# Kernel optimization log

Hardware: AMD Instinct MI355X
Metric: run time of the kernel (lower is better)

The kernel has to match this reference:

```python
import jax, jax.numpy as jnp
import numpy as np

B, S, D_IN, D_HID, D_OUT = 8, 2048, 1024, 1024, 1024


def setup_inputs() -> dict:
    key = jax.random.key(0)
    ks = jax.random.split(key, 11)
    def lin(kw, kb, fan_in, fan_out):
        bound = 1.0 / np.sqrt(fan_in)
        W = jax.random.uniform(kw, (fan_out, fan_in), minval=-bound, maxval=bound, dtype=jnp.float32)
        b = jax.random.uniform(kb, (fan_out,), minval=-bound, maxval=bound, dtype=jnp.float32)
        return W, b
    Wq, bq = lin(ks[0], ks[1], D_IN, D_HID)
    Wk, bk = lin(ks[2], ks[3], D_IN, D_HID)
    Wv, bv = lin(ks[4], ks[5], D_IN, D_HID)
    Wo, bo = lin(ks[6], ks[7], D_HID, D_OUT)
    gamma = jnp.ones((D_OUT,), jnp.float32)
    beta = jnp.zeros((D_OUT,), jnp.float32)
    x = jax.random.normal(ks[8], (B, S, D_IN), dtype=jnp.float32)
    return {"x": x, "Wq": Wq, "bq": bq, "Wk": Wk, "bk": bk,
            "Wv": Wv, "bv": bv, "Wo": Wo, "bo": bo,
            "gamma": gamma, "beta": beta}


def _layer_norm(x, gamma, beta, eps=1e-5):
    mu = jnp.mean(x, axis=-1, keepdims=True)
    var = jnp.var(x, axis=-1, keepdims=True)
    return (x - mu) * jax.lax.rsqrt(var + eps) * gamma + beta


def reference(x, Wq, bq, Wk, bk, Wv, bv, Wo, bo, gamma, beta):
    q = jnp.einsum('bsd,hd->bsh', x, Wq) + bq   # [B,S,H]
    k = jnp.einsum('bsd,hd->bsh', x, Wk) + bk
    v = jnp.einsum('bsd,hd->bsh', x, Wv) + bv
    scale = 1.0 / jnp.sqrt(jnp.float32(D_HID))
    scores = jnp.einsum('bqh,bkh->bqk', q, k) * scale  # [B,S,S]
    attn = jax.nn.softmax(scores, axis=-1)
    weighted = jnp.einsum('bqk,bkh->bqh', attn, v)     # [B,S,H]
    out = jnp.einsum('bsh,oh->bso', weighted, Wo) + bo # [B,S,O]
    return _layer_norm(out + x, gamma, beta)
```

## Files before the change

### kernel.cpp

```cpp
#include <hip/hip_runtime.h>
#include <hip/hip_bf16.h>
#include <math.h>


typedef __bf16 bf16;
typedef unsigned char u8;
typedef __attribute__((ext_vector_type(8))) __bf16 bf16x8;
typedef __attribute__((ext_vector_type(4))) __bf16 bf16x4;
typedef __attribute__((ext_vector_type(8))) int i32x8;
typedef __attribute__((ext_vector_type(16))) float f32x16;

__device__ __forceinline__ void async16(const u8* g, u8* l) {
    __builtin_amdgcn_global_load_lds(
        (const __attribute__((address_space(1))) void*)g,
        (__attribute__((address_space(3))) void*)l, 16, 0, 0);
}

#define WAITCNT_VM(n) __builtin_amdgcn_s_waitcnt((15 << 8) | (7 << 4) | (n))

__device__ __forceinline__ u8 to_fp8(float v) {
    return (u8)(__builtin_amdgcn_cvt_pk_fp8_f32(v, v, 0, 0) & 0xFF);
}

__global__ __launch_bounds__(256) void cast_all(
    const float* __restrict__ x,
    const float* __restrict__ W0, const float* __restrict__ W1,
    const float* __restrict__ W2, const float* __restrict__ W3,
    const float* __restrict__ bq, const float* __restrict__ bk,
    u8* __restrict__ x8, u8* __restrict__ w8, float* __restrict__ bqk)
{
    const int b = blockIdx.x, t = threadIdx.x;
    if (b < 8192) {
        const int i = (b * 256 + t) * 8;
        float4 a = *(const float4*)(x + i);
        float4 c = *(const float4*)(x + i + 4);
        int lo = __builtin_amdgcn_cvt_pk_fp8_f32(a.x, a.y, 0, 0);
        lo = __builtin_amdgcn_cvt_pk_fp8_f32(a.z, a.w, lo, 1);
        int hi = __builtin_amdgcn_cvt_pk_fp8_f32(c.x, c.y, 0, 0);
        hi = __builtin_amdgcn_cvt_pk_fp8_f32(c.z, c.w, hi, 1);
        int2 o = { lo, hi };
        *(int2*)(x8 + i) = o;
    } else if (b < 10240) {
        const int bb = b - 8192;
        const int wsel = bb >> 9;
        const float* src = (wsel == 0) ? W0 : (wsel == 1) ? W1
                         : (wsel == 2) ? W2 : W3;
        const int i = ((bb & 511) * 256 + t) * 8;
        float4 a = *(const float4*)(src + i);
        float4 c = *(const float4*)(src + i + 4);
        int lo = __builtin_amdgcn_cvt_pk_fp8_f32(a.x, a.y, 0, 0);
        lo = __builtin_amdgcn_cvt_pk_fp8_f32(a.z, a.w, lo, 1);
        int hi = __builtin_amdgcn_cvt_pk_fp8_f32(c.x, c.y, 0, 0);
        hi = __builtin_amdgcn_cvt_pk_fp8_f32(c.z, c.w, hi, 1);
        int2 o = { lo, hi };
        *(int2*)(w8 + (size_t)wsel * 1048576 + i) = o;
    } else {
        const int i = t * 8;
        const float* s = (i < 1024) ? (bq + i) : (bk + i - 1024);
        float4 a = *(const float4*)s;
        float4 c = *(const float4*)(s + 4);
        *(float4*)(bqk + i) = a;
        *(float4*)(bqk + i + 4) = c;
    }
}

__global__ __launch_bounds__(512) void gemm_f8(
    const u8* __restrict__ A, long lda, long sA,
    const u8* __restrict__ B, long ldb, long sB,
    void* __restrict__ Cv, long ldc, long sC,
    const float* __restrict__ bias, int bias_mode,
    float scale, int c_mode, int K)
{
    __shared__ u8 lds[3][32768];

    const int gx = gridDim.x, gy = gridDim.y;
    const int slice = gx * gy;
    const int total = slice * gridDim.z;
    int flat = ((int)blockIdx.z * gy + (int)blockIdx.y) * gx + (int)blockIdx.x;
    if ((total & 7) == 0)
        flat = (flat & 7) * (total >> 3) + (flat >> 3);
    const int bz = flat / slice;
    const int rem = flat - bz * slice;
    const int by = rem / gx;
    const int bx = rem - by * gx;

    const int tid = threadIdx.x;
    const long tM = (long)by * 256;
    const long tN = (long)bx * 256;
    A += (long)bz * sA;
    B += (long)bz * sB;

    const int s = tid & 255;
    const int line0 = s >> 3;
    const int sch = (s & 7) ^ (line0 & 7);
    const int skb = (sch & 3) << 4;
    const int srofs = (sch & 4) ? 128 : 0;
    const u8* gsrc;
    long gstr;
    if (tid < 256) { gsrc = A + (tM + line0 + srofs) * lda + skb; gstr = lda; }
    else           { gsrc = B + (tN + line0 + srofs) * ldb + skb; gstr = ldb; }
    const int dbase = ((tid < 256) ? 0 : 16384) + s * 16;

    const int w = tid >> 6, lane = tid & 63;
    const int wr = w >> 2, wc = w & 3;
    const int r32 = lane & 31, kh = lane >> 5;
    const int xr = r32 & 7;

    int oA[4][2], oB[2][2];
    const int cbA = wr * 4;
    const int cbB = (wc >> 1) * 4;
#pragma unroll
    for (int q = 0; q < 4; q++) {
        const int lineA = q * 32 + r32;
        oA[q][0] = lineA * 128 + (((cbA + 2 * kh + 0) ^ xr) << 4);
        oA[q][1] = lineA * 128 + (((cbA + 2 * kh + 1) ^ xr) << 4);
    }
#pragma unroll
    for (int n = 0; n < 2; n++) {
        const int lineB = (wc & 1) * 64 + n * 32 + r32;
        oB[n][0] = 16384 + lineB * 128 + (((cbB + 2 * kh + 0) ^ xr) << 4);
        oB[n][1] = 16384 + lineB * 128 + (((cbB + 2 * kh + 1) ^ xr) << 4);
    }

    f32x16 acc[4][2] = {};

    const int T = K >> 6;

#pragma unroll
    for (int j = 0; j < 4; j++)
        async16(gsrc + (long)j * 32 * gstr, &lds[0][dbase + j * 4096]);
#pragma unroll
    for (int j = 0; j < 4; j++)
        async16(gsrc + 64 + (long)j * 32 * gstr, &lds[1][dbase + j * 4096]);

    union F { i32x8 v; int4 q2[2]; };

    int cur = 0;
    for (int t = 0; t < T; ++t) {
        if (t + 1 < T) WAITCNT_VM(4);
        else WAITCNT_VM(0);
        __builtin_amdgcn_s_barrier();

        const u8* cb = lds[cur];

        F a0, a1, b0, b1;
        a0.q2[0] = *(const int4*)&cb[oA[0][0]];
        a0.q2[1] = *(const int4*)&cb[oA[0][1]];
        a1.q2[0] = *(const int4*)&cb[oA[1][0]];
        a1.q2[1] = *(const int4*)&cb[oA[1][1]];
        b0.q2[0] = *(const int4*)&cb[oB[0][0]];
        b0.q2[1] = *(const int4*)&cb[oB[0][1]];
        b1.q2[0] = *(const int4*)&cb[oB[1][0]];
        b1.q2[1] = *(const int4*)&cb[oB[1][1]];
        __builtin_amdgcn_sched_barrier(0);

        F a2, a3;
        a2.q2[0] = *(const int4*)&cb[oA[2][0]];
        a2.q2[1] = *(const int4*)&cb[oA[2][1]];
        a3.q2[0] = *(const int4*)&cb[oA[3][0]];
        a3.q2[1] = *(const int4*)&cb[oA[3][1]];
        if (t + 2 < T) {
            int nb = cur + 2; if (nb >= 3) nb -= 3;
            u8* pn = lds[nb];
            const long ko = (long)(t + 2) << 6;
#pragma unroll
            for (int j = 0; j < 4; j++)
                async16(gsrc + ko + (long)j * 32 * gstr,
                        pn + dbase + j * 4096);
        }

        asm volatile("s_waitcnt lgkmcnt(4)" ::: "memory");
        __builtin_amdgcn_sched_barrier(0);
        __builtin_amdgcn_s_setprio(1);
        acc[0][0] = __builtin_amdgcn_mfma_scale_f32_32x32x64_f8f6f4(
            a0.v, b0.v, acc[0][0], 0, 0, 0, 0x7F7F7F7F, 0, 0x7F7F7F7F);
        acc[0][1] = __builtin_amdgcn_mfma_scale_f32_32x32x64_f8f6f4(
            a0.v, b1.v, acc[0][1], 0, 0, 0, 0x7F7F7F7F, 0, 0x7F7F7F7F);
        acc[1][0] = __builtin_amdgcn_mfma_scale_f32_32x32x64_f8f6f4(
            a1.v, b0.v, acc[1][0], 0, 0, 0, 0x7F7F7F7F, 0, 0x7F7F7F7F);
        acc[1][1] = __builtin_amdgcn_mfma_scale_f32_32x32x64_f8f6f4(
            a1.v, b1.v, acc[1][1], 0, 0, 0, 0x7F7F7F7F, 0, 0x7F7F7F7F);
        __builtin_amdgcn_s_setprio(0);

        asm volatile("s_waitcnt lgkmcnt(0)" ::: "memory");
        __builtin_amdgcn_sched_barrier(0);
        __builtin_amdgcn_s_setprio(1);
        acc[2][0] = __builtin_amdgcn_mfma_scale_f32_32x32x64_f8f6f4(
            a2.v, b0.v, acc[2][0], 0, 0, 0, 0x7F7F7F7F, 0, 0x7F7F7F7F);
        acc[2][1] = __builtin_amdgcn_mfma_scale_f32_32x32x64_f8f6f4(
            a2.v, b1.v, acc[2][1], 0, 0, 0, 0x7F7F7F7F, 0, 0x7F7F7F7F);
        acc[3][0] = __builtin_amdgcn_mfma_scale_f32_32x32x64_f8f6f4(
            a3.v, b0.v, acc[3][0], 0, 0, 0, 0x7F7F7F7F, 0, 0x7F7F7F7F);
        acc[3][1] = __builtin_amdgcn_mfma_scale_f32_32x32x64_f8f6f4(
            a3.v, b1.v, acc[3][1], 0, 0, 0, 0x7F7F7F7F, 0, 0x7F7F7F7F);
        __builtin_amdgcn_s_setprio(0);

        if (++cur >= 3) cur = 0;
    }

#pragma unroll
    for (int q = 0; q < 4; q++) {
#pragma unroll
        for (int n = 0; n < 2; n++) {
            const long gn = tN + wc * 64 + n * 32 + r32;
            const float bn = (bias_mode == 1) ? bias[gn] : 0.0f;
#pragma unroll
            for (int reg = 0; reg < 16; reg++) {
                const int rowf = (reg & 3) + 8 * (reg >> 2) + 4 * kh;
                const long gm = tM + wr * 128 + q * 32 + rowf;
                float v = acc[q][n][reg] * scale + bn;
                if (bias_mode == 2) v += bias[gm];
                if (c_mode == 0)
                    ((bf16*)Cv + (long)bz * sC)[gm * ldc + gn] = (bf16)v;
                else
                    ((u8*)Cv + (long)bz * sC)[gm * ldc + gn] = to_fp8(v);
            }
        }
    }
}

__global__ __launch_bounds__(256) void softmax_f8(
    const bf16* __restrict__ S, u8* __restrict__ P)
{
    const long row = blockIdx.x;
    const bf16* p = S + row * 2048;
    const int t = threadIdx.x;

    bf16x8 v = *(const bf16x8*)(p + t * 8);
    float f[8];
    float m = -3.0e38f;
#pragma unroll
    for (int i = 0; i < 8; i++) { f[i] = (float)v[i]; m = fmaxf(m, f[i]); }
    for (int o = 32; o; o >>= 1) m = fmaxf(m, __shfl_down(m, o));

    __shared__ float sm[4], ssum[4];
    if ((t & 63) == 0) sm[t >> 6] = m;
    __syncthreads();
    m = fmaxf(fmaxf(sm[0], sm[1]), fmaxf(sm[2], sm[3]));

    float s = 0.0f;
#pragma unroll
    for (int i = 0; i < 8; i++) { f[i] = __expf(f[i] - m); s += f[i]; }
    for (int o = 32; o; o >>= 1) s += __shfl_down(s, o);
    if ((t & 63) == 0) ssum[t >> 6] = s;
    __syncthreads();
    s = ssum[0] + ssum[1] + ssum[2] + ssum[3];

    const float c = 256.0f / s;
    int lo = __builtin_amdgcn_cvt_pk_fp8_f32(f[0] * c, f[1] * c, 0, 0);
    lo = __builtin_amdgcn_cvt_pk_fp8_f32(f[2] * c, f[3] * c, lo, 1);
    int hi = __builtin_amdgcn_cvt_pk_fp8_f32(f[4] * c, f[5] * c, 0, 0);
    hi = __builtin_amdgcn_cvt_pk_fp8_f32(f[6] * c, f[7] * c, hi, 1);
    int2 o = { lo, hi };
    *(int2*)(P + row * 2048 + t * 8) = o;
}

__global__ __launch_bounds__(256) void ln_res(
    const bf16* __restrict__ pre, const float* __restrict__ x,
    const float* __restrict__ gamma, const float* __restrict__ beta,
    float* __restrict__ out)
{
    const long row = blockIdx.x;
    const int t = threadIdx.x;
    const long base = row * 1024 + t * 4;

    bf16x4 a = *(const bf16x4*)(pre + base);
    float4 b = *(const float4*)(x + base);
    float v0 = (float)a[0] + b.x, v1 = (float)a[1] + b.y;
    float v2 = (float)a[2] + b.z, v3 = (float)a[3] + b.w;

    float s = v0 + v1 + v2 + v3;
    float q = v0 * v0 + v1 * v1 + v2 * v2 + v3 * v3;
    for (int o = 32; o; o >>= 1) { s += __shfl_down(s, o); q += __shfl_down(q, o); }

    __shared__ float ls[4], lq[4];
    if ((t & 63) == 0) { ls[t >> 6] = s; lq[t >> 6] = q; }
    __syncthreads();
    s = ls[0] + ls[1] + ls[2] + ls[3];
    q = lq[0] + lq[1] + lq[2] + lq[3];

    const float mean = s * (1.0f / 1024.0f);
    const float var = q * (1.0f / 1024.0f) - mean * mean;
    const float rstd = rsqrtf(var + 1e-5f);

    const int c = t * 4;
    float4 g = *(const float4*)(gamma + c);
    float4 be = *(const float4*)(beta + c);
    float4 o;
    o.x = (v0 - mean) * rstd * g.x + be.x;
    o.y = (v1 - mean) * rstd * g.y + be.y;
    o.z = (v2 - mean) * rstd * g.z + be.z;
    o.w = (v3 - mean) * rstd * g.w + be.w;
    *(float4*)(out + base) = o;
}

extern "C" void kernel_launch(void* const* d_in, const int* in_sizes, int n_in,
                              void* d_out, int out_size, void* d_ws, size_t ws_size,
                              hipStream_t stream)
{
    const float* x     = (const float*)d_in[0];
    const float* Wq    = (const float*)d_in[1];
    const float* bq    = (const float*)d_in[2];
    const float* Wk    = (const float*)d_in[3];
    const float* bk    = (const float*)d_in[4];
    const float* Wv    = (const float*)d_in[5];
    const float* bv    = (const float*)d_in[6];
    const float* Wo    = (const float*)d_in[7];
    const float* bo    = (const float*)d_in[8];
    const float* gamma = (const float*)d_in[9];
    const float* beta  = (const float*)d_in[10];
    float* out = (float*)d_out;

    char* ws = (char*)d_ws;
    u8* x8  = (u8*)(ws + (size_t)0);
    u8* QK8 = (u8*)(ws + (size_t)16777216);
    u8* VT8 = (u8*)(ws + (size_t)50331648);
    u8* P8  = (u8*)(ws + (size_t)67108864);
    float* bqk = (float*)(ws + (size_t)100663296);
    bf16* Sb = (bf16*)(ws + (size_t)104857600);
    u8* Wq8 = (u8*)(ws + (size_t)176160768);
    u8* Wv8 = Wq8 + 2097152;
    u8* Wo8 = Wv8 + 1048576;
    u8* AO8 = x8;

    cast_all<<<10241, 256, 0, stream>>>(x, Wq, Wk, Wv, Wo, bq, bk,
                                        x8, Wq8, bqk);

    gemm_f8<<<dim3(8, 64, 1), 512, 0, stream>>>(
        x8, 1024, 0, Wq8, 1024, 0, (void*)QK8, 2048, 0, bqk, 1, 1.0f, 1, 1024);
    gemm_f8<<<dim3(64, 4, 1), 512, 0, stream>>>(
        Wv8, 1024, 0, x8, 1024, 0, (void*)VT8, 16384, 0, bv, 2, 1.0f, 1, 1024);
    gemm_f8<<<dim3(8, 8, 8), 512, 0, stream>>>(
        QK8, 2048, 4194304, QK8 + 1024, 2048, 4194304, (void*)Sb, 2048, 4194304,
        nullptr, 0, 0.03125f, 0, 1024);
    softmax_f8<<<16384, 256, 0, stream>>>(Sb, P8);
    gemm_f8<<<dim3(4, 8, 8), 512, 0, stream>>>(
        P8, 2048, 4194304, VT8, 16384, 2048, (void*)AO8, 1024, 2097152,
        nullptr, 0, 0.0625f, 1, 2048);
    gemm_f8<<<dim3(4, 64, 1), 512, 0, stream>>>(
        AO8, 1024, 0, Wo8, 1024, 0, (void*)Sb, 1024, 0, bo, 1, 0.0625f, 0, 1024);
    ln_res<<<16384, 256, 0, stream>>>((const bf16*)Sb, x, gamma, beta, out);
}
```

Baseline: 389.6 us.

## Switch fp8 GEMM to double-buffered K=128 tiles with interleaved LDS reads

The GEMM main loop moves from a triple-buffered K=64 pipeline to a double-buffered K=128 pipeline, using 64KB per stage with a new 128-byte-row swizzle. Each iteration issues the next tile's async loads right after the barrier, then interleaves LDS fragment reads for the second K half with MFMAs of the first. The goal is fewer barriers and waits per unit of K, and better overlap of LDS reads with MFMA. In exchange it uses more LDS (128KB), which may limit occupancy, and it waits for all global loads (vmcnt 0) at every step, so prefetch depth is one tile.

Measured after the change: 388.5 us. About the same (-0.3%).

```diff
diff --git a/kernel.cpp b/kernel.cpp
--- a/kernel.cpp
+++ b/kernel.cpp
@@ -17,6 +17,8 @@
 }
 
 #define WAITCNT_VM(n) __builtin_amdgcn_s_waitcnt((15 << 8) | (7 << 4) | (n))
+#define LGKM(n) asm volatile("s_waitcnt lgkmcnt(" #n ")" ::: "memory")
+#define SBAR() __builtin_amdgcn_sched_barrier(0)
 
 __device__ __forceinline__ u8 to_fp8(float v) {
     return (u8)(__builtin_amdgcn_cvt_pk_fp8_f32(v, v, 0, 0) & 0xFF);
@@ -71,7 +73,7 @@
     const float* __restrict__ bias, int bias_mode,
     float scale, int c_mode, int K)
 {
-    __shared__ u8 lds[3][32768];
+    __shared__ u8 lds[2][65536];
 
     const int gx = gridDim.x, gy = gridDim.y;
     const int slice = gx * gy;
@@ -91,86 +93,73 @@
     B += (long)bz * sB;
 
     const int s = tid & 255;
-    const int line0 = s >> 3;
-    const int sch = (s & 7) ^ (line0 & 7);
-    const int skb = (sch & 3) << 4;
-    const int srofs = (sch & 4) ? 128 : 0;
+    const int row0 = s >> 3;
+    const int sch = (s & 7) ^ (row0 & 7);
+    const int skb = sch << 4;
     const u8* gsrc;
     long gstr;
-    if (tid < 256) { gsrc = A + (tM + line0 + srofs) * lda + skb; gstr = lda; }
-    else           { gsrc = B + (tN + line0 + srofs) * ldb + skb; gstr = ldb; }
-    const int dbase = ((tid < 256) ? 0 : 16384) + s * 16;
+    if (tid < 256) { gsrc = A + (tM + row0) * lda + skb; gstr = lda; }
+    else           { gsrc = B + (tN + row0) * ldb + skb; gstr = ldb; }
+    const int dbase = ((tid < 256) ? 0 : 32768) + s * 16;
 
     const int w = tid >> 6, lane = tid & 63;
     const int wr = w >> 2, wc = w & 3;
     const int r32 = lane & 31, kh = lane >> 5;
     const int xr = r32 & 7;
 
-    int oA[4][2], oB[2][2];
-    const int cbA = wr * 4;
-    const int cbB = (wc >> 1) * 4;
-#pragma unroll
-    for (int q = 0; q < 4; q++) {
-        const int lineA = q * 32 + r32;
-        oA[q][0] = lineA * 128 + (((cbA + 2 * kh + 0) ^ xr) << 4);
-        oA[q][1] = lineA * 128 + (((cbA + 2 * kh + 1) ^ xr) << 4);
-    }
-#pragma unroll
-    for (int n = 0; n < 2; n++) {
-        const int lineB = (wc & 1) * 64 + n * 32 + r32;
-        oB[n][0] = 16384 + lineB * 128 + (((cbB + 2 * kh + 0) ^ xr) << 4);
-        oB[n][1] = 16384 + lineB * 128 + (((cbB + 2 * kh + 1) ^ xr) << 4);
-    }
+    const int dk = (xr & 4) ? -64 : 64;
+    const int dp = (xr & 1) ? -16 : 16;
+    const int cb0 = ((2 * kh) ^ xr) << 4;
+    int oA[4], oB[2];
+#pragma unroll
+    for (int q = 0; q < 4; q++)
+        oA[q] = (wr * 128 + q * 32 + r32) * 128 + cb0;
+#pragma unroll
+    for (int n = 0; n < 2; n++)
+        oB[n] = 32768 + (wc * 64 + n * 32 + r32) * 128 + cb0;
 
     f32x16 acc[4][2] = {};
 
-    const int T = K >> 6;
-
-#pragma unroll
-    for (int j = 0; j < 4; j++)
+    const int T = K >> 7;
+
+#pragma unroll
+    for (int j = 0; j < 8; j++)
         async16(gsrc + (long)j * 32 * gstr, &lds[0][dbase + j * 4096]);
-#pragma unroll
-    for (int j = 0; j < 4; j++)
-        async16(gsrc + 64 + (long)j * 32 * gstr, &lds[1][dbase + j * 4096]);
 
     union F { i32x8 v; int4 q2[2]; };
 
-    int cur = 0;
     for (int t = 0; t < T; ++t) {
-        if (t + 1 < T) WAITCNT_VM(4);
-        else WAITCNT_VM(0);
+        WAITCNT_VM(0);
         __builtin_amdgcn_s_barrier();
 
-        const u8* cb = lds[cur];
-
-        F a0, a1, b0, b1;
-        a0.q2[0] = *(const int4*)&cb[oA[0][0]];
-        a0.q2[1] = *(const int4*)&cb[oA[0][1]];
-        a1.q2[0] = *(const int4*)&cb[oA[1][0]];
-        a1.q2[1] = *(const int4*)&cb[oA[1][1]];
-        b0.q2[0] = *(const int4*)&cb[oB[0][0]];
-        b0.q2[1] = *(const int4*)&cb[oB[0][1]];
-        b1.q2[0] = *(const int4*)&cb[oB[1][0]];
-        b1.q2[1] = *(const int4*)&cb[oB[1][1]];
-        __builtin_amdgcn_sched_barrier(0);
-
-        F a2, a3;
-        a2.q2[0] = *(const int4*)&cb[oA[2][0]];
-        a2.q2[1] = *(const int4*)&cb[oA[2][1]];
-        a3.q2[0] = *(const int4*)&cb[oA[3][0]];
-        a3.q2[1] = *(const int4*)&cb[oA[3][1]];
-        if (t + 2 < T) {
-            int nb = cur + 2; if (nb >= 3) nb -= 3;
-            u8* pn = lds[nb];
-            const long ko = (long)(t + 2) << 6;
-#pragma unroll
-            for (int j = 0; j < 4; j++)
+        if (t + 1 < T) {
+            u8* pn = lds[(t + 1) & 1];
+            const long ko = (long)(t + 1) << 7;
+#pragma unroll
+            for (int j = 0; j < 8; j++)
                 async16(gsrc + ko + (long)j * 32 * gstr,
                         pn + dbase + j * 4096);
         }
 
-        asm volatile("s_waitcnt lgkmcnt(4)" ::: "memory");
-        __builtin_amdgcn_sched_barrier(0);
+        const u8* cb = lds[t & 1];
+
+        F a0, a1, b0, b1, a2, a3;
+        a0.q2[0] = *(const int4*)&cb[oA[0]];
+        a0.q2[1] = *(const int4*)&cb[oA[0] + dp];
+        a1.q2[0] = *(const int4*)&cb[oA[1]];
+        a1.q2[1] = *(const int4*)&cb[oA[1] + dp];
+        b0.q2[0] = *(const int4*)&cb[oB[0]];
+        b0.q2[1] = *(const int4*)&cb[oB[0] + dp];
+        b1.q2[0] = *(const int4*)&cb[oB[1]];
+        b1.q2[1] = *(const int4*)&cb[oB[1] + dp];
+        SBAR();
+        a2.q2[0] = *(const int4*)&cb[oA[2]];
+        a2.q2[1] = *(const int4*)&cb[oA[2] + dp];
+        a3.q2[0] = *(const int4*)&cb[oA[3]];
+        a3.q2[1] = *(const int4*)&cb[oA[3] + dp];
+        SBAR();
+
+        LGKM(4); SBAR();
         __builtin_amdgcn_s_setprio(1);
         acc[0][0] = __builtin_amdgcn_mfma_scale_f32_32x32x64_f8f6f4(
             a0.v, b0.v, acc[0][0], 0, 0, 0, 0x7F7F7F7F, 0, 0x7F7F7F7F);
@@ -181,9 +170,20 @@
         acc[1][1] = __builtin_amdgcn_mfma_scale_f32_32x32x64_f8f6f4(
             a1.v, b1.v, acc[1][1], 0, 0, 0, 0x7F7F7F7F, 0, 0x7F7F7F7F);
         __builtin_amdgcn_s_setprio(0);
-
-        asm volatile("s_waitcnt lgkmcnt(0)" ::: "memory");
-        __builtin_amdgcn_sched_barrier(0);
+        SBAR();
+
+        F c0, c1, d0, d1;
+        c0.q2[0] = *(const int4*)&cb[oA[0] + dk];
+        c0.q2[1] = *(const int4*)&cb[oA[0] + dk + dp];
+        c1.q2[0] = *(const int4*)&cb[oA[1] + dk];
+        c1.q2[1] = *(const int4*)&cb[oA[1] + dk + dp];
+        d0.q2[0] = *(const int4*)&cb[oB[0] + dk];
+        d0.q2[1] = *(const int4*)&cb[oB[0] + dk + dp];
+        d1.q2[0] = *(const int4*)&cb[oB[1] + dk];
+        d1.q2[1] = *(const int4*)&cb[oB[1] + dk + dp];
+        SBAR();
+
+        LGKM(8); SBAR();
         __builtin_amdgcn_s_setprio(1);
         acc[2][0] = __builtin_amdgcn_mfma_scale_f32_32x32x64_f8f6f4(
             a2.v, b0.v, acc[2][0], 0, 0, 0, 0x7F7F7F7F, 0, 0x7F7F7F7F);
@@ -194,8 +194,40 @@
         acc[3][1] = __builtin_amdgcn_mfma_scale_f32_32x32x64_f8f6f4(
             a3.v, b1.v, acc[3][1], 0, 0, 0, 0x7F7F7F7F, 0, 0x7F7F7F7F);
         __builtin_amdgcn_s_setprio(0);
-
-        if (++cur >= 3) cur = 0;
+        SBAR();
+
+        F c2, c3;
+        c2.q2[0] = *(const int4*)&cb[oA[2] + dk];
+        c2.q2[1] = *(const int4*)&cb[oA[2] + dk + dp];
+        c3.q2[0] = *(const int4*)&cb[oA[3] + dk];
+        c3.q2[1] = *(const int4*)&cb[oA[3] + dk + dp];
+        SBAR();
+
+        LGKM(4); SBAR();
+        __builtin_amdgcn_s_setprio(1);
+        acc[0][0] = __builtin_amdgcn_mfma_scale_f32_32x32x64_f8f6f4(
+            c0.v, d0.v, acc[0][0], 0, 0, 0, 0x7F7F7F7F, 0, 0x7F7F7F7F);
+        acc[0][1] = __builtin_amdgcn_mfma_scale_f32_32x32x64_f8f6f4(
+            c0.v, d1.v, acc[0][1], 0, 0, 0, 0x7F7F7F7F, 0, 0x7F7F7F7F);
+        acc[1][0] = __builtin_amdgcn_mfma_scale_f32_32x32x64_f8f6f4(
+            c1.v, d0.v, acc[1][0], 0, 0, 0, 0x7F7F7F7F, 0, 0x7F7F7F7F);
+        acc[1][1] = __builtin_amdgcn_mfma_scale_f32_32x32x64_f8f6f4(
+            c1.v, d1.v, acc[1][1], 0, 0, 0, 0x7F7F7F7F, 0, 0x7F7F7F7F);
+        __builtin_amdgcn_s_setprio(0);
+        SBAR();
+
+        LGKM(0); SBAR();
+        __builtin_amdgcn_s_setprio(1);
+        acc[2][0] = __builtin_amdgcn_mfma_scale_f32_32x32x64_f8f6f4(
+            c2.v, d0.v, acc[2][0], 0, 0, 0, 0x7F7F7F7F, 0, 0x7F7F7F7F);
+        acc[2][1] = __builtin_amdgcn_mfma_scale_f32_32x32x64_f8f6f4(
+            c2.v, d1.v, acc[2][1], 0, 0, 0, 0x7F7F7F7F, 0, 0x7F7F7F7F);
+        acc[3][0] = __builtin_amdgcn_mfma_scale_f32_32x32x64_f8f6f4(
+            c3.v, d0.v, acc[3][0], 0, 0, 0, 0x7F7F7F7F, 0, 0x7F7F7F7F);
+        acc[3][1] = __builtin_amdgcn_mfma_scale_f32_32x32x64_f8f6f4(
+            c3.v, d1.v, acc[3][1], 0, 0, 0, 0x7F7F7F7F, 0, 0x7F7F7F7F);
+        __builtin_amdgcn_s_setprio(0);
+        SBAR();
     }
 
 #pragma unroll
```
